# Optimization experiments

Measured on AMD Instinct MI355X. Metric: run time of the kernel, lower is better.

Reference implementation:

```python
import jax, jax.numpy as jnp
import numpy as np

B, NUM_REF, FDIM, H, W, D = 2, 3, 256, 64, 64, 10
GAMMA = 0.5


def setup_inputs() -> dict:
    key = jax.random.key(0)
    k1, k2, k3, k4 = jax.random.split(key, 4)
    ref = jax.random.normal(k1, (B, NUM_REF, FDIM, H, W), jnp.float32)
    target = jax.random.normal(k2, (B, FDIM, H, W), jnp.float32)
    # one-hot reference labels, class axis = 2, per docstring
    lab = jax.random.randint(k3, (B, NUM_REF, H, W), 0, D)
    ref_label = jax.nn.one_hot(lab, D, axis=2, dtype=jnp.float32)  # (B,NUM_REF,D,H,W)
    target_label = jax.random.randint(k4, (B, H, W), 0, D)
    return {
        "ref": ref,
        "target": target,
        "ref_label": ref_label,
        "target_label": target_label,
        "unused1": 0,
        "unused2": 0,
    }


def reference(ref, target, ref_label, target_label, unused1, unused2):
    b, n, f, h, w = ref.shape
    # similarity: (B, num_ref*H*W, H*W)
    r = jnp.transpose(ref, (0, 1, 3, 4, 2)).reshape(b, n * h * w, f)
    t = target.reshape(b, f, h * w)
    sim = jnp.einsum('brf,bft->brt', r, t)
    sim = jax.nn.softmax(sim, axis=1)  # softmax over reference pixels
    # label propagation: (B, d, H*W)
    d = ref_label.shape[2]
    rl = jnp.transpose(ref_label, (0, 2, 1, 3, 4)).reshape(b, d, n * h * w)
    pred = jnp.einsum('bdr,brt->bdt', rl, sim)  # (B, d, Nt)
    # flatten to (B*H*W, d), matching torch permute(0,2,3,1).reshape(-1,c)
    pred = jnp.transpose(pred, (0, 2, 1)).reshape(-1, d)
    tl = target_label.reshape(-1)
    log_p = jax.nn.log_softmax(pred, axis=-1)
    log_pt = jnp.take_along_axis(log_p, tl[:, None], axis=1)[:, 0]  # (B*H*W,)
    ce = -jnp.mean(log_pt)  # nn.NLLLoss default mean -> scalar
    focal_term = (1.0 - jnp.exp(log_pt)) ** GAMMA  # per-pixel
    loss = jnp.mean(focal_term * ce)  # vector * scalar, then mean
    return loss
```

## Files before the change

### kernel.cpp

```cpp
#include <hip/hip_runtime.h>
#include <hip/hip_bf16.h>
#include <stdint.h>
#include <stddef.h>

#define B_    2
#define NREF  3
#define FDIM  256
#define HW    4096
#define DCLS  10
#define RTOT  12288
#define TT    128
#define RR    64
#define RS    8
#define RPB   1536
#define NCH   24
#define NPIX  8192
#define LOG2E 1.44269504f
#define C0f   (-144.269504f)

typedef __attribute__((ext_vector_type(8))) short bf16x8;
typedef __attribute__((ext_vector_type(4))) float f32x4;
typedef __attribute__((ext_vector_type(4))) unsigned int u32x4;

__device__ __forceinline__ unsigned short f2bf(float x) {
  union { float f; unsigned u; } v; v.f = x;
  unsigned r = v.u + 0x7fffu + ((v.u >> 16) & 1u);
  return (unsigned short)(r >> 16);
}
__device__ __forceinline__ unsigned pk2(float a, float b) {
  return (unsigned)f2bf(a) | ((unsigned)f2bf(b) << 16);
}
__device__ __forceinline__ unsigned cvtpk(float a, float b) {
  unsigned r;
  asm("v_cvt_pk_bf16_f32 %0, %1, %2" : "=v"(r) : "v"(a), "v"(b));
  return r;
}
__device__ __forceinline__ void async16(const void* g, void* l) {
  __builtin_amdgcn_global_load_lds(
      (const __attribute__((address_space(1))) void*)g,
      (__attribute__((address_space(3))) void*)l, 16, 0, 0);
}
__device__ __forceinline__ unsigned oh2(unsigned word, int d) {
  return ((word & 255u) == (unsigned)d ? 0x3F80u : 0u) |
         (((word >> 8) & 255u) == (unsigned)d ? 0x3F800000u : 0u);
}

__global__ __launch_bounds__(256) void k_pre(const float* __restrict__ ref,
                                             const float* __restrict__ tgt,
                                             const float* __restrict__ rl,
                                             char* __restrict__ outb,
                                             unsigned char* __restrict__ lab8) {
  const int tid = threadIdx.x;
  if (blockIdx.x < 512) {
    const int row = blockIdx.x * 64 + (tid & 63);
    const int q = tid >> 6;
    const float* src;
    float scl;
    if (row < B_ * RTOT) {
      const int b = row / RTOT, rr2 = row % RTOT;
      src = ref + ((size_t)(b * NREF + (rr2 >> 12)) * FDIM) * HW + (rr2 & 4095);
      scl = LOG2E;
    } else {
      const int r2 = row - B_ * RTOT;
      src = tgt + ((size_t)(r2 >> 12) * FDIM) * HW + (r2 & 4095);
      scl = 1.0f;
    }
    char* dst = outb + (size_t)row * 512;
    const int sw = (row & 7) << 4;
#pragma unroll
    for (int ci = 0; ci < 4; ++ci) {
      const int c16 = q * 4 + ci;
      float v[8];
#pragma unroll
      for (int j = 0; j < 8; ++j) v[j] = src[(size_t)(c16 * 8 + j) * HW] * scl;
      u32x4 u;
      u[0] = pk2(v[0], v[1]); u[1] = pk2(v[2], v[3]);
      u[2] = pk2(v[4], v[5]); u[3] = pk2(v[6], v[7]);
      *(u32x4*)(dst + ((c16 * 16) ^ sw)) = u;
    }
  } else {
    const int idx = (blockIdx.x - 512) * 256 + tid;
    if (idx >= B_ * RTOT) return;
    const int b = idx / RTOT, r = idx % RTOT;
    const float* p = rl + ((size_t)((b * NREF + (r >> 12)) * DCLS)) * HW + (r & 4095);
    int v = 0;
#pragma unroll
    for (int d = 1; d < DCLS; ++d)
      if (p[(size_t)d * HW] > 0.5f) v = d;
    lab8[idx] = (unsigned char)v;
  }
}

__global__ __launch_bounds__(256, 2) void k_main(const char* __restrict__ refb,
                                                 const char* __restrict__ tgtb,
                                                 const unsigned char* __restrict__ lab8,
                                                 float* __restrict__ pred) {
  __shared__ __align__(16) char Ash[2][RR * 512];

  const int tid = threadIdx.x;
  const int lane = tid & 63;
  const int w = tid >> 6;
  const int l15 = lane & 15, l4 = lane >> 4;
  const int rh = w >> 1, th = w & 1;
  const int swz = (l15 & 7) << 4;

  const int bid = blockIdx.x;
  const int rs = bid & 7;
  const int tb = (bid >> 3) & 31;
  const int b  = bid >> 8;

  bf16x8 bfr[4][8];
  {
    const char* base = tgtb + ((size_t)(b * HW + tb * TT + th * 64)) * 512;
#pragma unroll
    for (int nt = 0; nt < 4; ++nt) {
      const char* rp = base + (size_t)((nt * 16 + l15) * 512);
#pragma unroll
      for (int ks = 0; ks < 8; ++ks)
        bfr[nt][ks] = *(const bf16x8*)(rp + ((ks * 64 + l4 * 16) ^ swz));
    }
  }

  f32x4 pacc[4];
#pragma unroll
  for (int i = 0; i < 4; ++i) pacc[i] = f32x4{0.f, 0.f, 0.f, 0.f};

  const char* Asrc = refb + ((size_t)(b * RTOT + rs * RPB)) * 512;

  const char* ap00 = &Ash[0][(rh * 32 +  0 + l15) * 512 + ((     l4 * 16) ^ swz)];
  const char* ap01 = &Ash[0][(rh * 32 +  0 + l15) * 512 + ((64 + l4 * 16) ^ swz)];
  const char* ap10 = &Ash[0][(rh * 32 + 16 + l15) * 512 + ((     l4 * 16) ^ swz)];
  const char* ap11 = &Ash[0][(rh * 32 + 16 + l15) * 512 + ((64 + l4 * 16) ^ swz)];

  auto stage = [&](const char* s, char* dbuf) {
#pragma unroll
    for (int i2 = 0; i2 < 8; ++i2) {
      const int seg = i2 * 4 + w;
      async16(s + seg * 1024 + lane * 16, dbuf + seg * 1024);
    }
  };
  auto qk = [&](f32x4 (&acc)[2][4], const int OFS) {
#pragma unroll
    for (int i2 = 0; i2 < 2; ++i2)
#pragma unroll
      for (int j = 0; j < 4; ++j) acc[i2][j] = f32x4{C0f, C0f, C0f, C0f};
    __builtin_amdgcn_s_setprio(1);
#pragma unroll
    for (int ks = 0; ks < 8; ++ks) {
      const int ko = OFS + (ks >> 1) * 128;
      const bf16x8 af0 = *(const bf16x8*)(((ks & 1) ? ap01 : ap00) + ko);
      const bf16x8 af1 = *(const bf16x8*)(((ks & 1) ? ap11 : ap10) + ko);
#pragma unroll
      for (int nt = 0; nt < 4; ++nt)
        acc[0][nt] = __builtin_amdgcn_mfma_f32_16x16x32_bf16(
            af0, bfr[nt][ks], acc[0][nt], 0, 0, 0);
#pragma unroll
      for (int nt = 0; nt < 4; ++nt)
        acc[1][nt] = __builtin_amdgcn_mfma_f32_16x16x32_bf16(
            af1, bfr[nt][ks], acc[1][nt], 0, 0, 0);
    }
    __builtin_amdgcn_s_setprio(0);
  };
  auto pv = [&](const f32x4 (&acc)[2][4], unsigned la, unsigned lb2) {
    union { bf16x8 v; unsigned u[4]; } lf;
    lf.u[0] = oh2(la, l15);        lf.u[1] = oh2(la >> 16, l15);
    lf.u[2] = oh2(lb2, l15);       lf.u[3] = oh2(lb2 >> 16, l15);
#pragma unroll
    for (int nt = 0; nt < 4; ++nt) {
      const f32x4 a0 = acc[0][nt], a1 = acc[1][nt];
      float p0 = __builtin_amdgcn_exp2f(a0[0]);
      float p1 = __builtin_amdgcn_exp2f(a0[1]);
      float p2 = __builtin_amdgcn_exp2f(a0[2]);
      float p3 = __builtin_amdgcn_exp2f(a0[3]);
      float p4 = __builtin_amdgcn_exp2f(a1[0]);
      float p5 = __builtin_amdgcn_exp2f(a1[1]);
      float p6 = __builtin_amdgcn_exp2f(a1[2]);
      float p7 = __builtin_amdgcn_exp2f(a1[3]);
      union { bf16x8 v; unsigned u[4]; } pf;
      pf.u[0] = cvtpk(p0, p1); pf.u[1] = cvtpk(p2, p3);
      pf.u[2] = cvtpk(p4, p5); pf.u[3] = cvtpk(p6, p7);
      pacc[nt] = __builtin_amdgcn_mfma_f32_16x16x32_bf16(lf.v, pf.v, pacc[nt], 0, 0, 0);
    }
  };

  f32x4 accA[2][4], accB[2][4];
  const unsigned char* lbp = lab8 + b * RTOT + rs * RPB + rh * 32 + l4 * 4;
  const char* Acur = Asrc + 2 * (RR * 512);

  unsigned la_p = *(const unsigned*)lbp;
  unsigned lb_p = *(const unsigned*)(lbp + 16);
  lbp += RR;
  stage(Asrc, &Ash[0][0]);
  __syncthreads();
  stage(Asrc + RR * 512, &Ash[1][0]);
  qk(accA, 0);

#pragma unroll 1
  for (int i = 0; i < 11; ++i) {
    {
      __syncthreads();
      const unsigned la_n = *(const unsigned*)lbp;
      const unsigned lb_n = *(const unsigned*)(lbp + 16);
      lbp += RR;
      stage(Acur, &Ash[0][0]); Acur += RR * 512;
      pv(accA, la_p, lb_p);
      qk(accB, 32768);
      la_p = la_n; lb_p = lb_n;
    }
    {
      __syncthreads();
      const unsigned la_n = *(const unsigned*)lbp;
      const unsigned lb_n = *(const unsigned*)(lbp + 16);
      lbp += RR;
      stage(Acur, &Ash[1][0]); Acur += RR * 512;
      pv(accB, la_p, lb_p);
      qk(accA, 0);
      la_p = la_n; lb_p = lb_n;
    }
  }
  {
    __syncthreads();
    const unsigned la_n = *(const unsigned*)lbp;
    const unsigned lb_n = *(const unsigned*)(lbp + 16);
    pv(accA, la_p, lb_p);
    qk(accB, 32768);
    pv(accB, la_n, lb_n);
  }

  __syncthreads();
  float* sc = (float*)&Ash[0][0];
  if (rh == 1) {
#pragma unroll
    for (int nt = 0; nt < 4; ++nt)
      *(f32x4*)&sc[((th * 64 + lane) * 4 + nt) * 4] = pacc[nt];
  }
  __syncthreads();
  if (rh == 0) {
#pragma unroll
    for (int nt = 0; nt < 4; ++nt) {
      pacc[nt] += *(const f32x4*)&sc[((th * 64 + lane) * 4 + nt) * 4];
      const int t = th * 64 + nt * 16 + l15;
      const size_t o = (((size_t)(rs * B_ + b)) * HW + (size_t)tb * TT + t) * 16 + l4 * 4;
      *(f32x4*)&pred[o] = pacc[nt];
    }
  }
}

__global__ __launch_bounds__(256) void k_epi(const float* __restrict__ pred,
                                             const int* __restrict__ tl,
                                             float* __restrict__ red) {
  const int idx = blockIdx.x * 256 + threadIdx.x;
  const int b = idx >> 12, t = idx & 4095;
  union { f32x4 v[3]; float f[12]; } S;
  S.v[0] = f32x4{0.f, 0.f, 0.f, 0.f};
  S.v[1] = f32x4{0.f, 0.f, 0.f, 0.f};
  S.v[2] = f32x4{0.f, 0.f, 0.f, 0.f};
#pragma unroll
  for (int r = 0; r < RS; ++r) {
    const f32x4* p = (const f32x4*)&pred[(((size_t)(r * B_ + b)) * HW + t) * 16];
    S.v[0] += p[0]; S.v[1] += p[1]; S.v[2] += p[2];
  }
  float T = 0.f;
#pragma unroll
  for (int d = 0; d < DCLS; ++d) T += S.f[d];
  const float inv = 1.f / T;
  const int lb = tl[idx];
  float se = 0.f, zt = 0.f;
#pragma unroll
  for (int d = 0; d < DCLS; ++d) {
    const float z = S.f[d] * inv;
    se += __expf(z);
    if (d == lb) zt = z;
  }
  const float logpt = zt - __logf(se);
  const float pt = __expf(zt) / se;
  const float focal = sqrtf(fmaxf(1.f - pt, 0.f));

  float lp = logpt, fo = focal;
#pragma unroll
  for (int off = 32; off; off >>= 1) {
    lp += __shfl_down(lp, off);
    fo += __shfl_down(fo, off);
  }
  __shared__ float rb_[8];
  const int lane = threadIdx.x & 63, wv = threadIdx.x >> 6;
  if (lane == 0) { rb_[wv] = lp; rb_[4 + wv] = fo; }
  __syncthreads();
  if (threadIdx.x == 0) {
    red[blockIdx.x * 2 + 0] = rb_[0] + rb_[1] + rb_[2] + rb_[3];
    red[blockIdx.x * 2 + 1] = rb_[4] + rb_[5] + rb_[6] + rb_[7];
  }
}

__global__ void k_fin(const float* __restrict__ red, float* __restrict__ out) {
  const int tid = threadIdx.x;
  float lp = 0.f, fo = 0.f;
  if (tid < 32) { lp = red[tid * 2]; fo = red[tid * 2 + 1]; }
#pragma unroll
  for (int off = 16; off; off >>= 1) {
    lp += __shfl_down(lp, off);
    fo += __shfl_down(fo, off);
  }
  if (tid == 0) {
    const float ce = -lp / (float)NPIX;
    out[0] = ce * (fo / (float)NPIX);
  }
}

extern "C" void kernel_launch(void* const* d_in, const int* in_sizes, int n_in,
                              void* d_out, int out_size, void* d_ws, size_t ws_size,
                              hipStream_t stream)
{
  const float* ref  = (const float*)d_in[0];
  const float* tgt  = (const float*)d_in[1];
  const float* rl   = (const float*)d_in[2];
  const int*   tlab = (const int*)d_in[3];
  float* out = (float*)d_out;

  char* ws = (char*)d_ws;
  char* refb = ws;
  char* tgtb = ws + (size_t)24576 * 512;
  unsigned char* lab8 = (unsigned char*)(ws + 16777216);
  float* pred = (float*)(ws + 16777216 + 32768);
  float* red  = (float*)(ws + 16777216 + 32768 + 4194304);

  k_pre<<<608, 256, 0, stream>>>(ref, tgt, rl, refb, lab8);
  k_main<<<512, 256, 0, stream>>>(refb, tgtb, lab8, pred);
  k_epi<<<32, 256, 0, stream>>>(pred, tlab, red);
  k_fin<<<1, 64, 0, stream>>>(red, out);
}
```

Baseline: 59.14 us.

## Give each warp private reference slices, drop block barriers, double grid

The main attention kernel now gives each block 64 target pixels instead of 128, doubling the grid to 1024 blocks. Each warp owns a private 16-row slice of every reference chunk, so staging waits only on that warp's own async loads via vmcnt rather than on block-wide __syncthreads. Labels are prefetched once into shared memory. This cuts barrier stalls and raises occupancy, but each block now loads the reference data for fewer target pixels, doubling total reference traffic, and the final reduction now sums across four warps.

```diff
diff --git a/kernel.cpp b/kernel.cpp
--- a/kernel.cpp
+++ b/kernel.cpp
@@ -9,7 +9,6 @@
 #define HW    4096
 #define DCLS  10
 #define RTOT  12288
-#define TT    128
 #define RR    64
 #define RS    8
 #define RPB   1536
@@ -44,6 +43,11 @@
   return ((word & 255u) == (unsigned)d ? 0x3F80u : 0u) |
          (((word >> 8) & 255u) == (unsigned)d ? 0x3F800000u : 0u);
 }
+#define WAIT_VMCNT(N)                                          \
+  do {                                                         \
+    asm volatile("s_waitcnt vmcnt(" #N ")" ::: "memory");      \
+    __builtin_amdgcn_sched_barrier(0);                         \
+  } while (0)
 
 __global__ __launch_bounds__(256) void k_pre(const float* __restrict__ ref,
                                              const float* __restrict__ tgt,
@@ -95,23 +99,23 @@
                                                  const char* __restrict__ tgtb,
                                                  const unsigned char* __restrict__ lab8,
                                                  float* __restrict__ pred) {
-  __shared__ __align__(16) char Ash[2][RR * 512];
+  __shared__ __align__(16) char Ash[2][32768];
+  __shared__ __align__(16) char Lsh[4][2048];
 
   const int tid = threadIdx.x;
   const int lane = tid & 63;
   const int w = tid >> 6;
   const int l15 = lane & 15, l4 = lane >> 4;
-  const int rh = w >> 1, th = w & 1;
   const int swz = (l15 & 7) << 4;
 
   const int bid = blockIdx.x;
   const int rs = bid & 7;
-  const int tb = (bid >> 3) & 31;
-  const int b  = bid >> 8;
+  const int tb = (bid >> 3) & 63;
+  const int b  = bid >> 9;
 
   bf16x8 bfr[4][8];
   {
-    const char* base = tgtb + ((size_t)(b * HW + tb * TT + th * 64)) * 512;
+    const char* base = tgtb + ((size_t)(b * HW + tb * 64)) * 512;
 #pragma unroll
     for (int nt = 0; nt < 4; ++nt) {
       const char* rp = base + (size_t)((nt * 16 + l15) * 512);
@@ -127,55 +131,46 @@
 
   const char* Asrc = refb + ((size_t)(b * RTOT + rs * RPB)) * 512;
 
-  const char* ap00 = &Ash[0][(rh * 32 +  0 + l15) * 512 + ((     l4 * 16) ^ swz)];
-  const char* ap01 = &Ash[0][(rh * 32 +  0 + l15) * 512 + ((64 + l4 * 16) ^ swz)];
-  const char* ap10 = &Ash[0][(rh * 32 + 16 + l15) * 512 + ((     l4 * 16) ^ swz)];
-  const char* ap11 = &Ash[0][(rh * 32 + 16 + l15) * 512 + ((64 + l4 * 16) ^ swz)];
-
-  auto stage = [&](const char* s, char* dbuf) {
-#pragma unroll
-    for (int i2 = 0; i2 < 8; ++i2) {
-      const int seg = i2 * 4 + w;
-      async16(s + seg * 1024 + lane * 16, dbuf + seg * 1024);
-    }
+  const char* ap0 = &Ash[0][w * 8192 + l15 * 512 + ((     l4 * 16) ^ swz)];
+  const char* ap1 = &Ash[0][w * 8192 + l15 * 512 + ((64 + l4 * 16) ^ swz)];
+
+  auto stage = [&](int c) {
+    const char* s = Asrc + (size_t)c * 32768 + w * 8192;
+    char* d = &Ash[c & 1][w * 8192];
+#pragma unroll
+    for (int i2 = 0; i2 < 8; ++i2)
+      async16(s + i2 * 1024 + lane * 16, d + i2 * 1024);
   };
-  auto qk = [&](f32x4 (&acc)[2][4], const int OFS) {
-#pragma unroll
-    for (int i2 = 0; i2 < 2; ++i2)
-#pragma unroll
-      for (int j = 0; j < 4; ++j) acc[i2][j] = f32x4{C0f, C0f, C0f, C0f};
+  auto qk = [&](f32x4 (&acc)[4], const int OFS) {
+#pragma unroll
+    for (int j = 0; j < 4; ++j) acc[j] = f32x4{C0f, C0f, C0f, C0f};
     __builtin_amdgcn_s_setprio(1);
 #pragma unroll
     for (int ks = 0; ks < 8; ++ks) {
       const int ko = OFS + (ks >> 1) * 128;
-      const bf16x8 af0 = *(const bf16x8*)(((ks & 1) ? ap01 : ap00) + ko);
-      const bf16x8 af1 = *(const bf16x8*)(((ks & 1) ? ap11 : ap10) + ko);
+      const bf16x8 af = *(const bf16x8*)(((ks & 1) ? ap1 : ap0) + ko);
 #pragma unroll
       for (int nt = 0; nt < 4; ++nt)
-        acc[0][nt] = __builtin_amdgcn_mfma_f32_16x16x32_bf16(
-            af0, bfr[nt][ks], acc[0][nt], 0, 0, 0);
-#pragma unroll
-      for (int nt = 0; nt < 4; ++nt)
-        acc[1][nt] = __builtin_amdgcn_mfma_f32_16x16x32_bf16(
-            af1, bfr[nt][ks], acc[1][nt], 0, 0, 0);
+        acc[nt] = __builtin_amdgcn_mfma_f32_16x16x32_bf16(
+            af, bfr[nt][ks], acc[nt], 0, 0, 0);
     }
     __builtin_amdgcn_s_setprio(0);
   };
-  auto pv = [&](const f32x4 (&acc)[2][4], unsigned la, unsigned lb2) {
+  auto pv = [&](const f32x4 (&aE)[4], const f32x4 (&aO)[4],
+                unsigned laE, unsigned laO) {
     union { bf16x8 v; unsigned u[4]; } lf;
-    lf.u[0] = oh2(la, l15);        lf.u[1] = oh2(la >> 16, l15);
-    lf.u[2] = oh2(lb2, l15);       lf.u[3] = oh2(lb2 >> 16, l15);
+    lf.u[0] = oh2(laE, l15);        lf.u[1] = oh2(laE >> 16, l15);
+    lf.u[2] = oh2(laO, l15);        lf.u[3] = oh2(laO >> 16, l15);
 #pragma unroll
     for (int nt = 0; nt < 4; ++nt) {
-      const f32x4 a0 = acc[0][nt], a1 = acc[1][nt];
-      float p0 = __builtin_amdgcn_exp2f(a0[0]);
-      float p1 = __builtin_amdgcn_exp2f(a0[1]);
-      float p2 = __builtin_amdgcn_exp2f(a0[2]);
-      float p3 = __builtin_amdgcn_exp2f(a0[3]);
-      float p4 = __builtin_amdgcn_exp2f(a1[0]);
-      float p5 = __builtin_amdgcn_exp2f(a1[1]);
-      float p6 = __builtin_amdgcn_exp2f(a1[2]);
-      float p7 = __builtin_amdgcn_exp2f(a1[3]);
+      float p0 = __builtin_amdgcn_exp2f(aE[nt][0]);
+      float p1 = __builtin_amdgcn_exp2f(aE[nt][1]);
+      float p2 = __builtin_amdgcn_exp2f(aE[nt][2]);
+      float p3 = __builtin_amdgcn_exp2f(aE[nt][3]);
+      float p4 = __builtin_amdgcn_exp2f(aO[nt][0]);
+      float p5 = __builtin_amdgcn_exp2f(aO[nt][1]);
+      float p6 = __builtin_amdgcn_exp2f(aO[nt][2]);
+      float p7 = __builtin_amdgcn_exp2f(aO[nt][3]);
       union { bf16x8 v; unsigned u[4]; } pf;
       pf.u[0] = cvtpk(p0, p1); pf.u[1] = cvtpk(p2, p3);
       pf.u[2] = cvtpk(p4, p5); pf.u[3] = cvtpk(p6, p7);
@@ -183,64 +178,56 @@
     }
   };
 
-  f32x4 accA[2][4], accB[2][4];
-  const unsigned char* lbp = lab8 + b * RTOT + rs * RPB + rh * 32 + l4 * 4;
-  const char* Acur = Asrc + 2 * (RR * 512);
-
-  unsigned la_p = *(const unsigned*)lbp;
-  unsigned lb_p = *(const unsigned*)(lbp + 16);
-  lbp += RR;
-  stage(Asrc, &Ash[0][0]);
-  __syncthreads();
-  stage(Asrc + RR * 512, &Ash[1][0]);
+  {
+    const char* ls = (const char*)lab8 + b * RTOT + rs * RPB;
+    async16(ls + lane * 16, &Lsh[w][0]);
+    async16(ls + 1024 + lane * 16, &Lsh[w][1024]);
+  }
+  stage(0);
+  stage(1);
+  asm volatile("s_waitcnt vmcnt(0)" ::: "memory");
+  __builtin_amdgcn_sched_barrier(0);
+
+  const char* lq = &Lsh[w][w * 16 + l4 * 4];
+
+  f32x4 accA[4], accB[4];
   qk(accA, 0);
+  unsigned laE = *(const unsigned*)(lq);
+  unsigned laO = *(const unsigned*)(lq + 64);
 
 #pragma unroll 1
   for (int i = 0; i < 11; ++i) {
-    {
-      __syncthreads();
-      const unsigned la_n = *(const unsigned*)lbp;
-      const unsigned lb_n = *(const unsigned*)(lbp + 16);
-      lbp += RR;
-      stage(Acur, &Ash[0][0]); Acur += RR * 512;
-      pv(accA, la_p, lb_p);
-      qk(accB, 32768);
-      la_p = la_n; lb_p = lb_n;
-    }
-    {
-      __syncthreads();
-      const unsigned la_n = *(const unsigned*)lbp;
-      const unsigned lb_n = *(const unsigned*)(lbp + 16);
-      lbp += RR;
-      stage(Acur, &Ash[1][0]); Acur += RR * 512;
-      pv(accB, la_p, lb_p);
-      qk(accA, 0);
-      la_p = la_n; lb_p = lb_n;
-    }
-  }
-  {
-    __syncthreads();
-    const unsigned la_n = *(const unsigned*)lbp;
-    const unsigned lb_n = *(const unsigned*)(lbp + 16);
-    pv(accA, la_p, lb_p);
+    stage(2 * i + 2);
+    WAIT_VMCNT(8);
     qk(accB, 32768);
-    pv(accB, la_n, lb_n);
-  }
+    pv(accA, accB, laE, laO);
+    laE = *(const unsigned*)(lq + (2 * i + 2) * 64);
+    laO = *(const unsigned*)(lq + (2 * i + 3) * 64);
+    stage(2 * i + 3);
+    WAIT_VMCNT(8);
+    qk(accA, 0);
+  }
+  asm volatile("s_waitcnt vmcnt(0)" ::: "memory");
+  __builtin_amdgcn_sched_barrier(0);
+  qk(accB, 32768);
+  pv(accA, accB, laE, laO);
 
   __syncthreads();
   float* sc = (float*)&Ash[0][0];
-  if (rh == 1) {
+  if (w > 0) {
 #pragma unroll
     for (int nt = 0; nt < 4; ++nt)
-      *(f32x4*)&sc[((th * 64 + lane) * 4 + nt) * 4] = pacc[nt];
+      *(f32x4*)&sc[((w - 1) * 64 + lane) * 16 + nt * 4] = pacc[nt];
   }
   __syncthreads();
-  if (rh == 0) {
+  if (w == 0) {
 #pragma unroll
     for (int nt = 0; nt < 4; ++nt) {
-      pacc[nt] += *(const f32x4*)&sc[((th * 64 + lane) * 4 + nt) * 4];
-      const int t = th * 64 + nt * 16 + l15;
-      const size_t o = (((size_t)(rs * B_ + b)) * HW + (size_t)tb * TT + t) * 16 + l4 * 4;
+#pragma unroll
+      for (int ww = 0; ww < 3; ++ww)
+        pacc[nt] += *(const f32x4*)&sc[(ww * 64 + lane) * 16 + nt * 4];
+      const int t = tb * 64 + nt * 16 + l15;
+      const size_t o = (((size_t)(rs * B_ + b)) * HW + t) * 16 + l4 * 4;
       *(f32x4*)&pred[o] = pacc[nt];
     }
   }
@@ -325,7 +312,7 @@
   float* red  = (float*)(ws + 16777216 + 32768 + 4194304);
 
   k_pre<<<608, 256, 0, stream>>>(ref, tgt, rl, refb, lab8);
-  k_main<<<512, 256, 0, stream>>>(refb, tgtb, lab8, pred);
+  k_main<<<1024, 256, 0, stream>>>(refb, tgtb, lab8, pred);
   k_epi<<<32, 256, 0, stream>>>(pred, tlab, red);
   k_fin<<<1, 64, 0, stream>>>(red, out);
 }
```

New measurement: 66.96 us. 1.13x slower.
